# Kernel optimization log

Measured on AMD Instinct MI355X. Metric: run time of the kernel, lower is better.

Reference implementation:

```python
import jax, jax.numpy as jnp
import numpy as np

SCALE = 0.08838834764831845  # 1/sqrt(output_dim=128)


def setup_inputs() -> dict:
    key = jax.random.key(0)
    ks = jax.random.split(key, 7)
    N, D, H, E = 4096, 1024, 8, 128
    s = 0.02
    return {
        "X": jax.random.normal(ks[0], (N, D), jnp.float32),
        "Wq": jax.random.normal(ks[1], (H, D, E), jnp.float32) * s,
        "bq": jax.random.normal(ks[2], (H, E), jnp.float32) * s,
        "Wk": jax.random.normal(ks[3], (H, D, E), jnp.float32) * s,
        "bk": jax.random.normal(ks[4], (H, E), jnp.float32) * s,
        "Wv": jax.random.normal(ks[5], (H, D, E), jnp.float32) * s,
        "bv": jax.random.normal(ks[6], (H, E), jnp.float32) * s,
    }


def reference(X, Wq, bq, Wk, bk, Wv, bv):
    # per-head projections, batched over heads: [H, N, E]
    q = jnp.einsum("nd,hde->hne", X, Wq) + bq[:, None, :]
    k = jnp.einsum("nd,hde->hne", X, Wk) + bk[:, None, :]
    v = jnp.einsum("nd,hde->hne", X, Wv) + bv[:, None, :]
    # score[h, n, m] = scale * q[h,n,:] . k[h,m,:]  ([H, N, N])
    score = SCALE * jnp.einsum("hne,hme->hnm", q, k)
    # NOTE: original uses nn.Softmax(dim=0) on the [N, N] per-head matrix,
    # i.e. normalization over the QUERY (row) axis -> axis=1 here.
    attn = jax.nn.softmax(score, axis=1)
    # z[h, n, e] = sum_m attn[h,n,m] * v[h,m,e]
    z = jnp.einsum("hnm,hme->hne", attn, v)
    # concat heads along feature dim: [N, H*E]
    H, N, E = z.shape
    Z = jnp.transpose(z, (1, 0, 2)).reshape(N, H * E)
    return jax.nn.sigmoid(Z)
```

## Files before the change

### kernel.cpp

```cpp
#include <hip/hip_runtime.h>
#include <hip/hip_bf16.h>
#include <stdint.h>

typedef __bf16 bf16_t;
typedef __bf16 bf16x4 __attribute__((ext_vector_type(4)));
typedef __bf16 bf16x8 __attribute__((ext_vector_type(8)));
typedef float f32x4 __attribute__((ext_vector_type(4)));

#define MFMA_16x16x32(A, B, C) __builtin_amdgcn_mfma_f32_16x16x32_bf16(A, B, C, 0, 0, 0)
#define EXP2(x) __builtin_amdgcn_exp2f(x)

static constexpr float kScale = 0.08838834764831845f;
static constexpr float kLog2e = 1.4426950408889634f;
static constexpr float kC1 = kScale * kLog2e;

__device__ __forceinline__ void lds_cp16(void* lds, const void* g) {
  __builtin_amdgcn_global_load_lds(
      (__attribute__((address_space(1))) void*)(uintptr_t)g,
      (__attribute__((address_space(3))) void*)(uintptr_t)lds, 16, 0, 0);
}

template <int R, int K>
__device__ __forceinline__ void stage_tile(bf16_t* lds, const bf16_t* g, int ldg, int tid) {
  constexpr int TOT = R * K;
  constexpr int CH = R * 32;
  constexpr int ITERS = TOT / 2048;
  const int wave = tid >> 6;
#pragma unroll
  for (int i = 0; i < ITERS; ++i) {
    int linear = i * 2048 + tid * 8;
    int chunk = linear / CH;
    int rem = linear % CH;
    int r = rem >> 5;
    int c = rem & 31;
    lds_cp16(lds + i * 2048 + wave * 512, g + r * ldg + chunk * 32 + c);
  }
}

__device__ __forceinline__ bf16x8 frag_ld(const bf16_t* lds_chunk, int row, int lane) {
  return *(const bf16x8*)(lds_chunk + row * 32 + ((lane >> 4) << 3));
}

__global__ void cvt_kernel(const float* __restrict__ src, bf16_t* __restrict__ dst) {
  const int i = (blockIdx.x * 256 + threadIdx.x) * 4;
  float4 v = *(const float4*)&src[i];
  bf16x4 o;
  o[0] = (bf16_t)v.x;
  o[1] = (bf16_t)v.y;
  o[2] = (bf16_t)v.z;
  o[3] = (bf16_t)v.w;
  *(bf16x4*)&dst[i] = o;
}

__global__ void transpose_f32_k(const float* __restrict__ src, bf16_t* __restrict__ dst, int R,
                                int C) {
  __shared__ alignas(16) bf16_t tile[64][72];
  const int t = threadIdx.x;
  const int mat = blockIdx.z;
  const int r0 = blockIdx.x * 64, c0 = blockIdx.y * 64;
  const float* s = src + (size_t)mat * R * C;
  bf16_t* d = dst + (size_t)mat * R * C;
  const int rl = t >> 3, cl = (t & 7) * 8;
#pragma unroll
  for (int half = 0; half < 2; ++half) {
    const int r = r0 + rl + half * 32;
    float4 a = *(const float4*)&s[(size_t)r * C + c0 + cl];
    float4 b = *(const float4*)&s[(size_t)r * C + c0 + cl + 4];
    tile[cl + 0][rl + half * 32] = (bf16_t)a.x;
    tile[cl + 1][rl + half * 32] = (bf16_t)a.y;
    tile[cl + 2][rl + half * 32] = (bf16_t)a.z;
    tile[cl + 3][rl + half * 32] = (bf16_t)a.w;
    tile[cl + 4][rl + half * 32] = (bf16_t)b.x;
    tile[cl + 5][rl + half * 32] = (bf16_t)b.y;
    tile[cl + 6][rl + half * 32] = (bf16_t)b.z;
    tile[cl + 7][rl + half * 32] = (bf16_t)b.w;
  }
  __syncthreads();
  const int cl2 = t >> 3, rl2 = (t & 7) * 8;
  *(bf16x8*)&d[(size_t)(c0 + cl2) * R + r0 + rl2] = *(const bf16x8*)&tile[cl2][rl2];
  *(bf16x8*)&d[(size_t)(c0 + cl2 + 32) * R + r0 + rl2] = *(const bf16x8*)&tile[cl2 + 32][rl2];
}

__global__ __launch_bounds__(256, 2) void proj_kernel(const bf16_t* __restrict__ X,
                                                      const bf16_t* __restrict__ Wt,
                                                      const float* __restrict__ bq,
                                                      const float* __restrict__ bk,
                                                      const float* __restrict__ bv,
                                                      bf16_t* __restrict__ qkv) {
  __shared__ alignas(16) char smem[34816];
  bf16_t* As = (bf16_t*)smem;
  bf16_t* Bs = (bf16_t*)(smem + 8192);
  const int t = threadIdx.x, lane = t & 63, w = t >> 6;
  const int l15 = lane & 15, quad = lane >> 4;
  const int ntile = blockIdx.x, mat = blockIdx.y;
  const bf16_t* a0 = X + (size_t)ntile * 128 * 1024;
  const bf16_t* b0 = Wt + (size_t)mat * 131072;
  f32x4 acc[4][4] = {};
  const int rb = (w >> 1) * 64, cb = (w & 1) * 64;
  for (int k0 = 0; k0 < 1024; k0 += 32) {
    stage_tile<128, 32>(As, a0 + k0, 1024, t);
    stage_tile<128, 32>(Bs, b0 + k0, 1024, t);
    __syncthreads();
    bf16x8 af[4], bfr[4];
#pragma unroll
    for (int i = 0; i < 4; ++i) af[i] = frag_ld(As, rb + i * 16 + l15, lane);
#pragma unroll
    for (int j = 0; j < 4; ++j) bfr[j] = frag_ld(Bs, cb + j * 16 + l15, lane);
#pragma unroll
    for (int i = 0; i < 4; ++i)
#pragma unroll
      for (int j = 0; j < 4; ++j) acc[i][j] = MFMA_16x16x32(af[i], bfr[j], acc[i][j]);
    __syncthreads();
  }
  const int proj = mat >> 3, h = mat & 7;
  const float* bias = (proj == 0 ? bq : proj == 1 ? bk : bv) + h * 128;
  bf16_t* Ct = (bf16_t*)smem;
  bf16_t* dst = qkv + (size_t)proj * 4194304 + (size_t)h * 524288;
  if (proj < 2) {
#pragma unroll
    for (int i = 0; i < 4; ++i)
#pragma unroll
      for (int j = 0; j < 4; ++j) {
        const int e = cb + j * 16 + l15;
        const float bval = bias[e];
#pragma unroll
        for (int r = 0; r < 4; ++r)
          Ct[(rb + i * 16 + quad * 4 + r) * 136 + e] = (bf16_t)(acc[i][j][r] + bval);
      }
    __syncthreads();
#pragma unroll
    for (int u = 0; u < 2; ++u) {
      const int nt = w * 2 + u;
#pragma unroll
      for (int ks = 0; ks < 4; ++ks) {
        bf16x8 f = *(const bf16x8*)&Ct[(nt * 16 + l15) * 136 + ks * 32 + quad * 8];
        *(bf16x8*)&dst[(((size_t)(ntile * 8 + nt)) * 4 + ks) * 512 + lane * 8] = f;
      }
    }
  } else {
#pragma unroll
    for (int i = 0; i < 4; ++i)
#pragma unroll
      for (int j = 0; j < 4; ++j) {
        const int e = cb + j * 16 + l15;
        const float bval = bias[e];
        bf16x4 pv;
#pragma unroll
        for (int r = 0; r < 4; ++r) pv[r] = (bf16_t)(acc[i][j][r] + bval);
        *(bf16x4*)&Ct[e * 136 + rb + i * 16 + quad * 4] = pv;
      }
    __syncthreads();
#pragma unroll
    for (int es = 0; es < 8; ++es) {
      bf16x8 f = *(const bf16x8*)&Ct[(es * 16 + l15) * 136 + w * 32 + quad * 8];
      *(bf16x8*)&dst[(((size_t)(ntile * 4 + w)) * 8 + es) * 512 + lane * 8] = f;
    }
  }
}

__global__ __launch_bounds__(256, 2) void pass_a_kernel(const bf16_t* __restrict__ Qf,
                                                        const bf16_t* __restrict__ Kf,
                                                        float* __restrict__ l2c) {
  __shared__ alignas(16) float csred[4][64];
  const int t = threadIdx.x, lane = t & 63, w = t >> 6;
  const int l15 = lane & 15;
  const int h = blockIdx.x, mtile = blockIdx.y;
  const bf16_t* Qh = Qf + (size_t)h * 524288;
  const bf16_t* Kh = Kf + (size_t)h * 524288;
  bf16x8 kf[16];
#pragma unroll
  for (int mg = 0; mg < 4; ++mg)
#pragma unroll
    for (int ks = 0; ks < 4; ++ks)
      kf[mg * 4 + ks] = *(const bf16x8*)&Kh[((mtile * 4 + mg) * 4 + ks) * 512 + lane * 8];
  float cs[4] = {0.f, 0.f, 0.f, 0.f};
  uint32_t qo = w * 2048 + lane * 8;
  bf16x8 af[4];
#pragma unroll
  for (int ks = 0; ks < 4; ++ks) af[ks] = *(const bf16x8*)&Qh[qo + ks * 512];
  for (int it = 0; it < 64; ++it) {
    f32x4 c[4] = {};
#pragma unroll
    for (int ks = 0; ks < 4; ++ks)
#pragma unroll
      for (int mg = 0; mg < 4; ++mg) c[mg] = MFMA_16x16x32(af[ks], kf[mg * 4 + ks], c[mg]);
    qo += 8192;
#pragma unroll
    for (int ks = 0; ks < 4; ++ks) af[ks] = *(const bf16x8*)&Qh[qo + ks * 512];
#pragma unroll
    for (int mg = 0; mg < 4; ++mg)
#pragma unroll
      for (int r = 0; r < 4; ++r) cs[mg] += EXP2(c[mg][r] * kC1);
  }
#pragma unroll
  for (int mg = 0; mg < 4; ++mg) {
    cs[mg] += __shfl_xor(cs[mg], 16, 64);
    cs[mg] += __shfl_xor(cs[mg], 32, 64);
  }
  if (lane < 16) {
#pragma unroll
    for (int mg = 0; mg < 4; ++mg) csred[w][mg * 16 + lane] = cs[mg];
  }
  __syncthreads();
  if (t < 64)
    l2c[(size_t)h * 4096 + mtile * 64 + t] =
        __builtin_log2f(csred[0][t] + csred[1][t] + csred[2][t] + csred[3][t]);
}

__global__ __launch_bounds__(512, 2) void pass_b_kernel(const bf16_t* __restrict__ Qf,
                                                        const bf16_t* __restrict__ Kf,
                                                        const bf16_t* __restrict__ Vf,
                                                        const float* __restrict__ l2c,
                                                        float* __restrict__ out) {
  __shared__ alignas(16) char smem[151552];
  const int t = threadIdx.x, lane = t & 63, w = t >> 6;
  const int quad = lane >> 4, l15 = lane & 15;
  const int npar = w & 3, mpar = w >> 2;
  const int h = blockIdx.x, ntile = blockIdx.y;
  const bf16_t* Kh = Kf + (size_t)h * 524288;
  const char* VhB = (const char*)(Vf + (size_t)h * 524288);
  const bf16_t* Qh = Qf + (size_t)h * 524288;
  const float* lb = l2c + (size_t)h * 4096;
  bf16_t* sW = (bf16_t*)(smem + 131072) + w * 1280;

#pragma unroll
  for (int j = 0; j < 8; ++j) {
    const int off = (w * 8 + j) * 1024;
    lds_cp16(smem + off, VhB + off + lane * 16);
  }
  bf16x8 qf[2][4];
#pragma unroll
  for (int nsub = 0; nsub < 2; ++nsub)
#pragma unroll
    for (int ks = 0; ks < 4; ++ks)
      qf[nsub][ks] =
          *(const bf16x8*)&Qh[((ntile * 8 + npar * 2 + nsub) * 4 + ks) * 512 + lane * 8];
  bf16x8 kf[8];
  {
    const bf16_t* kg = Kh + mpar * 4096;
#pragma unroll
    for (int u = 0; u < 8; ++u) kf[u] = *(const bf16x8*)&kg[u * 512 + lane * 8];
  }
  f32x4 gc0 = *(const f32x4*)&lb[mpar * 32 + quad * 4];
  f32x4 gc1 = *(const f32x4*)&lb[mpar * 32 + 16 + quad * 4];
  f32x4 zacc[2][8] = {};
  __syncthreads();

  for (int wnd = 0; wnd < 16; ++wnd) {
    const int cur = wnd & 1;
    if (wnd < 15) {
      char* vdst = smem + (cur ^ 1) * 65536;
      const char* vsrc = VhB + (size_t)(wnd + 1) * 65536;
#pragma unroll
      for (int j = 0; j < 8; ++j) {
        const int off = (w * 8 + j) * 1024;
        lds_cp16(vdst + off, vsrc + off + lane * 16);
      }
    }
    __builtin_amdgcn_sched_barrier(0);
#pragma unroll
    for (int sub = 0; sub < 4; ++sub) {
      const int it = wnd * 4 + sub;
      f32x4 cc[2][2] = {};
      __builtin_amdgcn_s_setprio(1);
#pragma unroll
      for (int ks = 0; ks < 4; ++ks)
#pragma unroll
        for (int ms = 0; ms < 2; ++ms)
#pragma unroll
          for (int nsub = 0; nsub < 2; ++nsub)
            cc[ms][nsub] = MFMA_16x16x32(kf[ms * 4 + ks], qf[nsub][ks], cc[ms][nsub]);
      __builtin_amdgcn_s_setprio(0);
      {
        const bf16_t* kg = Kh + (size_t)(it + 1) * 8192 + mpar * 4096;
#pragma unroll
        for (int u = 0; u < 8; ++u) kf[u] = *(const bf16x8*)&kg[u * 512 + lane * 8];
      }
#pragma unroll
      for (int ms = 0; ms < 2; ++ms) {
        const f32x4 g = ms ? gc1 : gc0;
#pragma unroll
        for (int nsub = 0; nsub < 2; ++nsub) {
          bf16x4 pv;
#pragma unroll
          for (int r = 0; r < 4; ++r) pv[r] = (bf16_t)EXP2(cc[ms][nsub][r] * kC1 - g[r]);
          *(bf16x4*)&sW[(nsub * 16 + l15) * 40 + ms * 16 + quad * 4] = pv;
        }
      }
      {
        const int stn = (it < 63 ? it + 1 : 63) * 2 + mpar;
        gc0 = *(const f32x4*)&lb[stn * 32 + quad * 4];
        gc1 = *(const f32x4*)&lb[stn * 32 + 16 + quad * 4];
      }
      bf16x8 pf[2];
#pragma unroll
      for (int nsub = 0; nsub < 2; ++nsub)
        pf[nsub] = *(const bf16x8*)&sW[(nsub * 16 + l15) * 40 + quad * 8];
      const bf16_t* vbase = (const bf16_t*)(smem + cur * 65536 + sub * 16384) + mpar * 4096;
      __builtin_amdgcn_s_setprio(1);
#pragma unroll
      for (int es = 0; es < 8; ++es) {
        bf16x8 vf = *(const bf16x8*)&vbase[es * 512 + lane * 8];
#pragma unroll
        for (int nsub = 0; nsub < 2; ++nsub)
          zacc[nsub][es] = MFMA_16x16x32(pf[nsub], vf, zacc[nsub][es]);
      }
      __builtin_amdgcn_s_setprio(0);
    }
    asm volatile("s_waitcnt vmcnt(8)" ::: "memory");
    __builtin_amdgcn_s_barrier();
  }
  float* red = (float*)smem;
  if (mpar == 1) {
#pragma unroll
    for (int nsub = 0; nsub < 2; ++nsub)
#pragma unroll
      for (int es = 0; es < 8; ++es)
        *(f32x4*)&red[npar * 4096 + (nsub * 8 + es) * 256 + lane * 4] = zacc[nsub][es];
  }
  __syncthreads();
  if (mpar == 0) {
#pragma unroll
    for (int nsub = 0; nsub < 2; ++nsub) {
#pragma unroll
      for (int es = 0; es < 8; ++es) {
        f32x4 o = *(const f32x4*)&red[npar * 4096 + (nsub * 8 + es) * 256 + lane * 4];
        const int e = es * 16 + l15;
#pragma unroll
        for (int r = 0; r < 4; ++r) {
          const int n = ntile * 128 + npar * 32 + nsub * 16 + quad * 4 + r;
          const float z = zacc[nsub][es][r] + o[r];
          out[(size_t)n * 1024 + h * 128 + e] = 1.f / (1.f + EXP2(-z * kLog2e));
        }
      }
    }
  }
}

extern "C" void kernel_launch(void* const* d_in, const int* in_sizes, int n_in, void* d_out,
                              int out_size, void* d_ws, size_t ws_size, hipStream_t stream) {
  (void)in_sizes;
  (void)n_in;
  (void)out_size;
  (void)ws_size;
  const float* X = (const float*)d_in[0];
  const float* Wq = (const float*)d_in[1];
  const float* bq = (const float*)d_in[2];
  const float* Wk = (const float*)d_in[3];
  const float* bk = (const float*)d_in[4];
  const float* Wv = (const float*)d_in[5];
  const float* bv = (const float*)d_in[6];
  float* out = (float*)d_out;
  char* ws = (char*)d_ws;
  bf16_t* Qf = (bf16_t*)(ws);
  bf16_t* Kf = (bf16_t*)(ws + 8388608);
  bf16_t* Vf = (bf16_t*)(ws + 16777216);
  bf16_t* Xb = (bf16_t*)(ws + 25165824);
  bf16_t* Wt = (bf16_t*)(ws + 33554432);
  float* l2c = (float*)(ws + 39845888);

  cvt_kernel<<<4096, 256, 0, stream>>>(X, Xb);
  transpose_f32_k<<<dim3(16, 2, 8), 256, 0, stream>>>(Wq, Wt + (size_t)0 * 8 * 131072, 1024, 128);
  transpose_f32_k<<<dim3(16, 2, 8), 256, 0, stream>>>(Wk, Wt + (size_t)1 * 8 * 131072, 1024, 128);
  transpose_f32_k<<<dim3(16, 2, 8), 256, 0, stream>>>(Wv, Wt + (size_t)2 * 8 * 131072, 1024, 128);
  proj_kernel<<<dim3(32, 24), 256, 0, stream>>>(Xb, Wt, bq, bk, bv, Qf);
  pass_a_kernel<<<dim3(8, 64), 256, 0, stream>>>(Qf, Kf, l2c);
  pass_b_kernel<<<dim3(8, 32), 512, 0, stream>>>(Qf, Kf, Vf, l2c, out);
}
```

Baseline: 235.9 us.

## Software-pipeline score MFMAs one step ahead and transpose P in registers

The score tile for the next step is computed one iteration ahead, so its MFMAs can overlap with the exp and PV MFMAs of the current step. The K prefetch distance grows to two steps. The LDS round-trip that turned P into the A-operand layout is replaced by packed bf16 conversion plus permlane32 swap and ds_swizzle register shuffles, which frees 20KB of LDS and drops one LDS store/load pair per step. In exchange, register pressure rises from the extra accumulators, and the last iteration prefetches K past the end of the head buffer.

```diff
diff --git a/kernel.cpp b/kernel.cpp
--- a/kernel.cpp
+++ b/kernel.cpp
@@ -39,6 +39,29 @@
 
 __device__ __forceinline__ bf16x8 frag_ld(const bf16_t* lds_chunk, int row, int lane) {
   return *(const bf16x8*)(lds_chunk + row * 32 + ((lane >> 4) << 3));
+}
+
+__device__ __forceinline__ bf16x8 p_transpose(f32x4 pa, f32x4 pb, bool hi16) {
+  uint32_t a0, a1, b0, b1;
+  asm("v_cvt_pk_bf16_f32 %0, %1, %2" : "=v"(a0) : "v"(pa[0]), "v"(pa[1]));
+  asm("v_cvt_pk_bf16_f32 %0, %1, %2" : "=v"(a1) : "v"(pa[2]), "v"(pa[3]));
+  asm("v_cvt_pk_bf16_f32 %0, %1, %2" : "=v"(b0) : "v"(pb[0]), "v"(pb[1]));
+  asm("v_cvt_pk_bf16_f32 %0, %1, %2" : "=v"(b1) : "v"(pb[2]), "v"(pb[3]));
+  asm("v_permlane32_swap_b32 %0, %1" : "+v"(a0), "+v"(b0));
+  asm("v_permlane32_swap_b32 %0, %1" : "+v"(a1), "+v"(b1));
+  uint32_t sX0 = (uint32_t)__builtin_amdgcn_ds_swizzle((int)a0, 0x401F);
+  uint32_t sX1 = (uint32_t)__builtin_amdgcn_ds_swizzle((int)b0, 0x401F);
+  uint32_t sY0 = (uint32_t)__builtin_amdgcn_ds_swizzle((int)a1, 0x401F);
+  uint32_t sY1 = (uint32_t)__builtin_amdgcn_ds_swizzle((int)b1, 0x401F);
+  union {
+    uint32_t u[4];
+    bf16x8 v;
+  } r;
+  r.u[0] = hi16 ? sX1 : a0;
+  r.u[1] = hi16 ? sY1 : a1;
+  r.u[2] = hi16 ? b0 : sX0;
+  r.u[3] = hi16 ? b1 : sY0;
+  return r.v;
 }
 
 __global__ void cvt_kernel(const float* __restrict__ src, bf16_t* __restrict__ dst) {
@@ -212,16 +235,16 @@
                                                         const bf16_t* __restrict__ Vf,
                                                         const float* __restrict__ l2c,
                                                         float* __restrict__ out) {
-  __shared__ alignas(16) char smem[151552];
+  __shared__ alignas(16) char smem[131072];
   const int t = threadIdx.x, lane = t & 63, w = t >> 6;
   const int quad = lane >> 4, l15 = lane & 15;
+  const bool hi16 = (lane & 16) != 0;
   const int npar = w & 3, mpar = w >> 2;
   const int h = blockIdx.x, ntile = blockIdx.y;
   const bf16_t* Kh = Kf + (size_t)h * 524288;
   const char* VhB = (const char*)(Vf + (size_t)h * 524288);
   const bf16_t* Qh = Qf + (size_t)h * 524288;
   const float* lb = l2c + (size_t)h * 4096;
-  bf16_t* sW = (bf16_t*)(smem + 131072) + w * 1280;
 
 #pragma unroll
   for (int j = 0; j < 8; ++j) {
@@ -246,6 +269,22 @@
   f32x4 zacc[2][8] = {};
   __syncthreads();
 
+  f32x4 ccp[2][2] = {};
+  __builtin_amdgcn_s_setprio(1);
+#pragma unroll
+  for (int ks = 0; ks < 4; ++ks)
+#pragma unroll
+    for (int ms = 0; ms < 2; ++ms)
+#pragma unroll
+      for (int nsub = 0; nsub < 2; ++nsub)
+        ccp[ms][nsub] = MFMA_16x16x32(kf[ms * 4 + ks], qf[nsub][ks], ccp[ms][nsub]);
+  __builtin_amdgcn_s_setprio(0);
+  {
+    const bf16_t* kg = Kh + 8192 + mpar * 4096;
+#pragma unroll
+    for (int u = 0; u < 8; ++u) kf[u] = *(const bf16x8*)&kg[u * 512 + lane * 8];
+  }
+
   for (int wnd = 0; wnd < 16; ++wnd) {
     const int cur = wnd & 1;
     if (wnd < 15) {
@@ -261,7 +300,7 @@
 #pragma unroll
     for (int sub = 0; sub < 4; ++sub) {
       const int it = wnd * 4 + sub;
-      f32x4 cc[2][2] = {};
+      f32x4 ccn[2][2] = {};
       __builtin_amdgcn_s_setprio(1);
 #pragma unroll
       for (int ks = 0; ks < 4; ++ks)
@@ -269,33 +308,28 @@
         for (int ms = 0; ms < 2; ++ms)
 #pragma unroll
           for (int nsub = 0; nsub < 2; ++nsub)
-            cc[ms][nsub] = MFMA_16x16x32(kf[ms * 4 + ks], qf[nsub][ks], cc[ms][nsub]);
+            ccn[ms][nsub] = MFMA_16x16x32(kf[ms * 4 + ks], qf[nsub][ks], ccn[ms][nsub]);
       __builtin_amdgcn_s_setprio(0);
       {
-        const bf16_t* kg = Kh + (size_t)(it + 1) * 8192 + mpar * 4096;
+        const bf16_t* kg = Kh + (size_t)(it + 2) * 8192 + mpar * 4096;
 #pragma unroll
         for (int u = 0; u < 8; ++u) kf[u] = *(const bf16x8*)&kg[u * 512 + lane * 8];
       }
-#pragma unroll
-      for (int ms = 0; ms < 2; ++ms) {
-        const f32x4 g = ms ? gc1 : gc0;
-#pragma unroll
-        for (int nsub = 0; nsub < 2; ++nsub) {
-          bf16x4 pv;
-#pragma unroll
-          for (int r = 0; r < 4; ++r) pv[r] = (bf16_t)EXP2(cc[ms][nsub][r] * kC1 - g[r]);
-          *(bf16x4*)&sW[(nsub * 16 + l15) * 40 + ms * 16 + quad * 4] = pv;
-        }
+      bf16x8 pf[2];
+#pragma unroll
+      for (int nsub = 0; nsub < 2; ++nsub) {
+        f32x4 pa, pb;
+#pragma unroll
+        for (int r = 0; r < 4; ++r) pa[r] = EXP2(ccp[0][nsub][r] * kC1 - gc0[r]);
+#pragma unroll
+        for (int r = 0; r < 4; ++r) pb[r] = EXP2(ccp[1][nsub][r] * kC1 - gc1[r]);
+        pf[nsub] = p_transpose(pa, pb, hi16);
       }
       {
         const int stn = (it < 63 ? it + 1 : 63) * 2 + mpar;
         gc0 = *(const f32x4*)&lb[stn * 32 + quad * 4];
         gc1 = *(const f32x4*)&lb[stn * 32 + 16 + quad * 4];
       }
-      bf16x8 pf[2];
-#pragma unroll
-      for (int nsub = 0; nsub < 2; ++nsub)
-        pf[nsub] = *(const bf16x8*)&sW[(nsub * 16 + l15) * 40 + quad * 8];
       const bf16_t* vbase = (const bf16_t*)(smem + cur * 65536 + sub * 16384) + mpar * 4096;
       __builtin_amdgcn_s_setprio(1);
 #pragma unroll
@@ -306,6 +340,10 @@
           zacc[nsub][es] = MFMA_16x16x32(pf[nsub], vf, zacc[nsub][es]);
       }
       __builtin_amdgcn_s_setprio(0);
+#pragma unroll
+      for (int ms = 0; ms < 2; ++ms)
+#pragma unroll
+        for (int nsub = 0; nsub < 2; ++nsub) ccp[ms][nsub] = ccn[ms][nsub];
     }
     asm volatile("s_waitcnt vmcnt(8)" ::: "memory");
     __builtin_amdgcn_s_barrier();
```

New measurement: 239.8 us. No clear change (+1.7%).
